# Performance work log

Measured on AMD Instinct MI355X. Metric: run time of the kernel, lower is better.

## Reference

```python
import jax, jax.numpy as jnp
import numpy as np

B, S, I, H, C = 32, 512, 768, 512, 10


def setup_inputs() -> dict:
    key = jax.random.key(0)
    ks = jax.random.split(key, 16)
    n = lambda k, shp, s=0.02: jax.random.normal(k, shp, dtype=jnp.float32) * s
    inp = {
        "sentence_embeds": jax.random.normal(ks[0], (B, S, I), dtype=jnp.float32),
        "Wenc": n(ks[1], (H, I)),
        "benc": jnp.zeros((H,), jnp.float32),
        "Wdec": n(ks[2], (H, H)),
        "bdec": jnp.zeros((H,), jnp.float32),
        "v": jax.random.uniform(ks[3], (H,), dtype=jnp.float32),
        "Wih_f": n(ks[4], (4 * H, 2 * I)),
        "Whh_f": n(ks[5], (4 * H, H)),
        "bih_f": jnp.zeros((4 * H,), jnp.float32),
        "bhh_f": jnp.zeros((4 * H,), jnp.float32),
        "Wih_b": n(ks[6], (4 * H, 2 * I)),
        "Whh_b": n(ks[7], (4 * H, H)),
        "bih_b": jnp.zeros((4 * H,), jnp.float32),
        "bhh_b": jnp.zeros((4 * H,), jnp.float32),
        "Wout": n(ks[8], (C, 2 * H)),
        "bout": jnp.zeros((C,), jnp.float32),
    }
    return inp


def _run_direction(embeds, enc_proj, Wdec, bdec, v, Wih, Whh, bih, bhh):
    # embeds: [B,S,I], enc_proj: [B,S,H]. Returns per-step hidden states [S,B,H].
    b = embeds.shape[0]
    h0 = jnp.zeros((b, H), embeds.dtype)
    c0 = jnp.zeros((b, H), embeds.dtype)

    def step(carry, x_t):
        h, c = carry
        # Bahdanau additive attention over all encoder positions
        dec = h @ Wdec.T + bdec                                   # [B,H]
        scores = jnp.einsum("h,bsh->bs", v, jnp.tanh(enc_proj + dec[:, None, :]))
        w = jax.nn.softmax(scores, axis=1)                        # [B,S]
        ctx = jnp.einsum("bs,bsi->bi", w, embeds)                 # [B,I]
        inp = jnp.concatenate([ctx, x_t], axis=1)                 # [B,2I]
        gates = inp @ Wih.T + h @ Whh.T + (bih + bhh)             # [B,4H]
        i, f, g, o = jnp.split(gates, 4, axis=1)                  # torch LSTM gate order
        c = jax.nn.sigmoid(f) * c + jax.nn.sigmoid(i) * jnp.tanh(g)
        h = jax.nn.sigmoid(o) * jnp.tanh(c)
        return (h, c), h

    xs = jnp.swapaxes(embeds, 0, 1)  # [S,B,I]
    _, hs = jax.lax.scan(step, (h0, c0), xs)
    return hs


def reference(sentence_embeds, Wenc, benc, Wdec, bdec, v, Wih_f, Whh_f, bih_f, bhh_f,
              Wih_b, Whh_b, bih_b, bhh_b, Wout, bout):
    # Encoder projection is loop-invariant in the original; compute once.
    enc_proj = sentence_embeds @ Wenc.T + benc  # [B,S,H]
    hs_f = _run_direction(sentence_embeds, enc_proj, Wdec, bdec, v, Wih_f, Whh_f, bih_f, bhh_f)
    hs_b = _run_direction(sentence_embeds[:, ::-1, :], enc_proj, Wdec, bdec, v, Wih_b, Whh_b, bih_b, bhh_b)
    hs_b = hs_b[::-1]                                             # align backward outputs to time order
    combined = jnp.concatenate([hs_f, hs_b], axis=-1)             # [S,B,2H]
    preds = combined @ Wout.T + bout                              # [S,B,C]
    return jnp.swapaxes(preds, 0, 1)                              # [B,S,C]
```

## Files before the change

### kernel.cpp

```cpp
#include <hip/hip_runtime.h>
#include <stdint.h>

#define DEVINL __device__ __forceinline__

constexpr int B_  = 32;
constexpr int S_  = 512;
constexpr int I_  = 768;
constexpr int H_  = 512;
constexpr int C_  = 10;
constexpr int R_  = 64;
constexpr int G4H = 2048;
constexpr int I2_ = 1536;

using bf16x8 = __attribute__((ext_vector_type(8))) short;
using f32x4  = __attribute__((ext_vector_type(4))) float;
typedef unsigned short u16;
typedef unsigned int   u32;

constexpr size_t OFF_TE   = 0;
constexpr size_t OFF_EMB  = OFF_TE   + (size_t)B_*S_*H_*2;
constexpr size_t OFF_WDEC = OFF_EMB  + (size_t)B_*S_*I_*2;
constexpr size_t OFF_WHH  = OFF_WDEC + (size_t)H_*H_*2;
constexpr size_t OFF_WIL  = OFF_WHH  + (size_t)2*G4H*H_*2;
constexpr size_t OFF_WIR  = OFF_WIL  + (size_t)2*G4H*I_*2;
constexpr size_t OFF_WENC = OFF_WIR  + (size_t)2*G4H*I_*2;
constexpr size_t OFF_H    = OFF_WENC + (size_t)H_*I_*2;
constexpr size_t OFF_C    = OFF_H    + (size_t)R_*H_*2;
constexpr size_t OFF_TD   = OFF_C    + (size_t)R_*H_*4;
constexpr size_t OFF_HWH  = OFF_TD   + (size_t)R_*H_*4;
constexpr size_t OFF_XW   = OFF_HWH  + (size_t)R_*G4H*4;
constexpr size_t OFF_CTX  = OFF_XW   + (size_t)R_*G4H*4;
constexpr size_t OFF_SUME = OFF_CTX  + (size_t)R_*I_*4;
constexpr size_t OFF_M    = OFF_SUME + 256;
constexpr size_t WS_NEED  = OFF_M + 256;

DEVINL float asf(u32 u){ union{u32 i; float f;} x; x.i=u; return x.f; }
DEVINL u32   asu(float f){ union{u32 i; float f;} x; x.f=f; return x.i; }
DEVINL float bf2f(u16 h){ return asf((u32)h << 16); }
DEVINL u16   f2bf(float f){ u32 u = asu(f); return (u16)((u + 0x7fffu + ((u>>16)&1u)) >> 16); }
DEVINL float frcp(float x){
#if __has_builtin(__builtin_amdgcn_rcpf)
  return __builtin_amdgcn_rcpf(x);
#else
  return 1.0f/x;
#endif
}
DEVINL float sigm(float x){ return frcp(1.0f + __expf(-x)); }

__global__ void k_setup(char* ws, const float* Wenc, const float* Wdec,
                        const float* Whh_f, const float* Whh_b,
                        const float* Wih_f, const float* Wih_b,
                        float* out){
  int tid = blockIdx.x*blockDim.x + threadIdx.x;
  int nth = gridDim.x*blockDim.x;
  for (int i = tid; i < B_*S_*C_; i += nth) out[i] = 0.f;
  u16* hB = (u16*)(ws+OFF_H);
  for (int i = tid; i < R_*H_; i += nth) hB[i] = 0;
  float* cS = (float*)(ws+OFF_C);
  for (int i = tid; i < R_*H_; i += nth) cS[i] = 0.f;
  float* mb = (float*)(ws+OFF_M);
  for (int i = tid; i < R_; i += nth) mb[i] = 0.f;
  u16* wd = (u16*)(ws+OFF_WDEC);
  for (int i = tid; i < H_*H_; i += nth) wd[i] = f2bf(Wdec[i]);
  u16* we = (u16*)(ws+OFF_WENC);
  for (int i = tid; i < H_*I_; i += nth) we[i] = f2bf(Wenc[i]);
  u16* wh = (u16*)(ws+OFF_WHH);
  for (int i = tid; i < G4H*H_; i += nth){
    wh[i] = f2bf(Whh_f[i]);
    wh[G4H*H_ + i] = f2bf(Whh_b[i]);
  }
  u16* wl = (u16*)(ws+OFF_WIL);
  u16* wr = (u16*)(ws+OFF_WIR);
  for (int i = tid; i < G4H*I_; i += nth){
    int n = i / I_, k = i - n*I_;
    wl[i]            = f2bf(Wih_f[n*I2_ + k]);
    wr[i]            = f2bf(Wih_f[n*I2_ + I_ + k]);
    wl[G4H*I_ + i]   = f2bf(Wih_b[n*I2_ + k]);
    wr[G4H*I_ + i]   = f2bf(Wih_b[n*I2_ + I_ + k]);
  }
}

__global__ void k_embconv(char* ws, const float* emb){
  u16* e = (u16*)(ws+OFF_EMB);
  int tid = blockIdx.x*blockDim.x + threadIdx.x;
  int nth = gridDim.x*blockDim.x;
  int n4 = (B_*S_*I_)/4;
  const float4* src = (const float4*)emb;
  ushort4* dst = (ushort4*)e;
  for (int i = tid; i < n4; i += nth){
    float4 x = src[i];
    ushort4 o;
    o.x = f2bf(x.x); o.y = f2bf(x.y); o.z = f2bf(x.z); o.w = f2bf(x.w);
    dst[i] = o;
  }
}

__global__ __launch_bounds__(256) void k_enc(char* ws, const float* benc){
  const u16* A = (const u16*)(ws+OFF_EMB);
  const u16* W = (const u16*)(ws+OFF_WENC);
  u16* Te = (u16*)(ws+OFF_TE);
  int wg = blockIdx.x;
  int mt = wg >> 3, ng = wg & 7;
  int wave = threadIdx.x >> 6, lane = threadIdx.x & 63;
  int m0 = mt*16, n0 = ng*64 + wave*16;
  int lr = lane & 15, lkb = (lane>>4)*8;
  const u16* ap = A + (size_t)(m0+lr)*I_ + lkb;
  const u16* bp = W + (size_t)(n0+lr)*I_ + lkb;
  f32x4 acc = {0.f,0.f,0.f,0.f};
  for (int k = 0; k < I_; k += 32){
    bf16x8 a = *(const bf16x8*)(ap + k);
    bf16x8 b = *(const bf16x8*)(bp + k);
    acc = __builtin_amdgcn_mfma_f32_16x16x32_bf16(a, b, acc, 0, 0, 0);
  }
  int row4 = (lane>>4)*4;
  #pragma unroll
  for (int q = 0; q < 4; q++){
    int rr = m0 + row4 + q, cc = n0 + lr;
    Te[(size_t)rr*H_ + cc] = f2bf(tanhf(acc[q] + benc[cc]));
  }
}

__global__ __launch_bounds__(256) void k_step1(char* ws, const float* bdec, int t){
  int wg = blockIdx.x;
  if (wg >= 288){
    int tid = (wg-288)*256 + threadIdx.x;
    float* ctx = (float*)(ws+OFF_CTX);
    for (int i = tid; i < R_*I_; i += 512) ctx[i] = 0.f;
    float* se = (float*)(ws+OFF_SUME);
    for (int i = tid; i < R_; i += 512) se[i] = 0.f;
    return;
  }
  int wave = threadIdx.x >> 6, lane = threadIdx.x & 63;
  int tile = wg*4 + wave;
  int lr = lane & 15, lkb = (lane>>4)*8, row4 = (lane>>4)*4;
  const u16* hB = (const u16*)(ws+OFF_H);
  f32x4 acc = {0.f,0.f,0.f,0.f};
  if (tile < 128){
    int m0 = (tile>>5)*16, n0 = (tile&31)*16;
    const u16* W = (const u16*)(ws+OFF_WDEC);
    const u16* ap = hB + (size_t)(m0+lr)*H_ + lkb;
    const u16* bp = W + (size_t)(n0+lr)*H_ + lkb;
    for (int k = 0; k < H_; k += 32){
      bf16x8 a = *(const bf16x8*)(ap + k);
      bf16x8 b = *(const bf16x8*)(bp + k);
      acc = __builtin_amdgcn_mfma_f32_16x16x32_bf16(a, b, acc, 0, 0, 0);
    }
    float* Td = (float*)(ws+OFF_TD);
    #pragma unroll
    for (int q = 0; q < 4; q++){
      int rr = m0 + row4 + q, cc = n0 + lr;
      Td[rr*H_ + cc] = tanhf(acc[q] + bdec[cc]);
    }
  } else if (tile < 640){
    int t2 = tile - 128; int dir = t2 >> 8; int t3 = t2 & 255;
    int m0 = dir*32 + (t3>>7)*16;
    int n0 = (t3 & 127)*16;
    const u16* W = (const u16*)(ws+OFF_WHH) + (size_t)dir*G4H*H_;
    const u16* ap = hB + (size_t)(m0+lr)*H_ + lkb;
    const u16* bp = W + (size_t)(n0+lr)*H_ + lkb;
    for (int k = 0; k < H_; k += 32){
      bf16x8 a = *(const bf16x8*)(ap + k);
      bf16x8 b = *(const bf16x8*)(bp + k);
      acc = __builtin_amdgcn_mfma_f32_16x16x32_bf16(a, b, acc, 0, 0, 0);
    }
    float* o = (float*)(ws+OFF_HWH);
    #pragma unroll
    for (int q = 0; q < 4; q++){
      int rr = m0 + row4 + q;
      o[(size_t)rr*G4H + n0 + lr] = acc[q];
    }
  } else {
    int t2 = tile - 640; int dir = t2 >> 8; int t3 = t2 & 255;
    int bbase = (t3>>7)*16;
    int n0 = (t3 & 127)*16;
    int trow = dir ? (S_-1-t) : t;
    const u16* E = (const u16*)(ws+OFF_EMB);
    const u16* W = (const u16*)(ws+OFF_WIR) + (size_t)dir*G4H*I_;
    const u16* ap = E + ((size_t)(bbase+lr)*S_ + trow)*I_ + lkb;
    const u16* bp = W + (size_t)(n0+lr)*I_ + lkb;
    for (int k = 0; k < I_; k += 32){
      bf16x8 a = *(const bf16x8*)(ap + k);
      bf16x8 b = *(const bf16x8*)(bp + k);
      acc = __builtin_amdgcn_mfma_f32_16x16x32_bf16(a, b, acc, 0, 0, 0);
    }
    float* o = (float*)(ws+OFF_XW);
    #pragma unroll
    for (int q = 0; q < 4; q++){
      int bb = bbase + row4 + q;
      o[(size_t)(dir*32+bb)*G4H + n0 + lr] = acc[q];
    }
  }
}

__global__ __launch_bounds__(512) void k_attn(char* ws, const float* v){
  int wg = blockIdx.x;
  int b = wg & 31, pair = wg >> 5;
  int s0A = pair*32, s0B = S_ - pair*32 - 32;
  int tid = threadIdx.x, lane = tid & 63, wave = tid >> 6;
  const u16* Te = (const u16*)(ws+OFF_TE);
  const float* Td = (const float*)(ws+OFF_TD);
  const float* mb = (const float*)(ws+OFF_M);
  __shared__ float ldsE[2][2][32];
  int h0 = lane*8;
  float tdf[8], tdb[8], va[8];
  #pragma unroll
  for (int j = 0; j < 8; j++){
    tdf[j] = Td[b*H_ + h0 + j];
    tdb[j] = Td[(32+b)*H_ + h0 + j];
    va[j]  = v[h0 + j];
  }
  float mF = mb[b], mB = mb[32+b];
  for (int r = wave; r < 64; r += 8){
    int ci = r >> 5, u = r & 31;
    int s = (ci ? s0B : s0A) + u;
    const uint4 tv = *(const uint4*)(Te + ((size_t)(b*S_ + s))*H_ + h0);
    u32 wv[4] = {tv.x, tv.y, tv.z, tv.w};
    float af = 0.f, ab = 0.f;
    #pragma unroll
    for (int q = 0; q < 4; q++){
      int j = 2*q;
      float te0 = asf(wv[q] << 16);
      float te1 = asf(wv[q] & 0xffff0000u);
      float d0f = fmaf(te0, tdf[j],   1.0f);
      float d0b = fmaf(te0, tdb[j],   1.0f);
      af = fmaf((te0+tdf[j])*frcp(d0f), va[j], af);
      ab = fmaf((te0+tdb[j])*frcp(d0b), va[j], ab);
      float d1f = fmaf(te1, tdf[j+1], 1.0f);
      float d1b = fmaf(te1, tdb[j+1], 1.0f);
      af = fmaf((te1+tdf[j+1])*frcp(d1f), va[j+1], af);
      ab = fmaf((te1+tdb[j+1])*frcp(d1b), va[j+1], ab);
    }
    #pragma unroll
    for (int off = 1; off < 64; off <<= 1){
      af += __shfl_xor(af, off);
      ab += __shfl_xor(ab, off);
    }
    float ef = __expf(fminf(fmaxf(af - mF, -80.f), 80.f));
    float eb = __expf(fminf(fmaxf(ab - mB, -80.f), 80.f));
    if (lane == 0){ ldsE[0][ci][u] = ef; ldsE[1][ci][u] = eb; }
  }
  __syncthreads();
  if (tid < 2){
    float s = 0.f;
    for (int ci = 0; ci < 2; ci++)
      for (int u = 0; u < 32; u++) s += ldsE[tid][ci][u];
    atomicAdd((float*)(ws+OFF_SUME) + tid*32 + b, s);
  }
  if (tid < 192){
    int i0 = tid*4;
    const u16* E = (const u16*)(ws+OFF_EMB);
    float cf[4] = {0.f,0.f,0.f,0.f}, cb[4] = {0.f,0.f,0.f,0.f};
    for (int hf = 0; hf < 2; hf++){
      int sbase = hf ? s0B : s0A;
      for (int u = 0; u < 32; u++){
        ushort4 x4 = *(const ushort4*)(E + ((size_t)(b*S_ + sbase + u))*I_ + i0);
        float wf = ldsE[0][hf][u];
        float wb = ldsE[1][1-hf][31-u];
        float x0 = bf2f(x4.x), x1 = bf2f(x4.y), x2 = bf2f(x4.z), x3 = bf2f(x4.w);
        cf[0] = fmaf(wf, x0, cf[0]); cf[1] = fmaf(wf, x1, cf[1]);
        cf[2] = fmaf(wf, x2, cf[2]); cf[3] = fmaf(wf, x3, cf[3]);
        cb[0] = fmaf(wb, x0, cb[0]); cb[1] = fmaf(wb, x1, cb[1]);
        cb[2] = fmaf(wb, x2, cb[2]); cb[3] = fmaf(wb, x3, cb[3]);
      }
    }
    float* ctx = (float*)(ws+OFF_CTX);
    #pragma unroll
    for (int z = 0; z < 4; z++){
      atomicAdd(&ctx[(size_t)b*I_ + i0 + z], cf[z]);
      atomicAdd(&ctx[(size_t)(32+b)*I_ + i0 + z], cb[z]);
    }
  }
}

__global__ __launch_bounds__(256) void k_upd(char* ws,
        const float* bih_f, const float* bhh_f,
        const float* bih_b, const float* bhh_b,
        const float* Wout, const float* bout,
        float* out, int t){
  int wg = blockIdx.x;
  int dir = wg >> 5, hc = wg & 31;
  int tid = threadIdx.x, lane = tid & 63, gt = tid >> 6;
  __shared__ u16 Abuf[32][776];
  __shared__ float Gs[4][32][16];
  __shared__ float Hb[32][16];
  __shared__ float ldsInv[32];
  const float* ctx = (const float*)(ws+OFF_CTX) + (size_t)dir*32*I_;
  const float* se  = (const float*)(ws+OFF_SUME) + dir*32;
  if (tid < 32) ldsInv[tid] = 1.0f / fmaxf(se[tid], 1e-30f);
  __syncthreads();
  for (int idx = tid; idx < 32*I_; idx += 256){
    int bb = idx / I_, k = idx - bb*I_;
    Abuf[bb][k] = f2bf(ctx[(size_t)bb*I_ + k] * ldsInv[bb]);
  }
  __syncthreads();
  int lr = lane & 15, lkb = (lane>>4)*8, row4 = (lane>>4)*4;
  const u16* W = (const u16*)(ws+OFF_WIL) + (size_t)dir*G4H*I_;
  int n_g = gt*512 + hc*16 + lr;
  const u16* bp = W + (size_t)n_g*I_ + lkb;
  f32x4 acc0 = {0.f,0.f,0.f,0.f}, acc1 = {0.f,0.f,0.f,0.f};
  for (int k = 0; k < I_; k += 32){
    bf16x8 av0 = *(const bf16x8*)(&Abuf[lr][k + lkb]);
    bf16x8 av1 = *(const bf16x8*)(&Abuf[16 + lr][k + lkb]);
    bf16x8 bv  = *(const bf16x8*)(bp + k);
    acc0 = __builtin_amdgcn_mfma_f32_16x16x32_bf16(av0, bv, acc0, 0, 0, 0);
    acc1 = __builtin_amdgcn_mfma_f32_16x16x32_bf16(av1, bv, acc1, 0, 0, 0);
  }
  const float* xW = (const float*)(ws+OFF_XW);
  const float* hW = (const float*)(ws+OFF_HWH);
  const float* bih = dir ? bih_b : bih_f;
  const float* bhh = dir ? bhh_b : bhh_f;
  #pragma unroll
  for (int q = 0; q < 4; q++){
    int bb = row4 + q; int rr = dir*32 + bb;
    Gs[gt][bb][lr] = acc0[q] + xW[(size_t)rr*G4H + n_g] + hW[(size_t)rr*G4H + n_g]
                   + bih[n_g] + bhh[n_g];
  }
  #pragma unroll
  for (int q = 0; q < 4; q++){
    int bb = 16 + row4 + q; int rr = dir*32 + bb;
    Gs[gt][bb][lr] = acc1[q] + xW[(size_t)rr*G4H + n_g] + hW[(size_t)rr*G4H + n_g]
                   + bih[n_g] + bhh[n_g];
  }
  __syncthreads();
  float* cS = (float*)(ws+OFF_C);
  u16* hB = (u16*)(ws+OFF_H);
  for (int ci = tid; ci < 512; ci += 256){
    int bb = ci >> 4, j = ci & 15;
    int hg = hc*16 + j, rr = dir*32 + bb;
    float ig = sigm(Gs[0][bb][j]);
    float fg = sigm(Gs[1][bb][j]);
    float gg = tanhf(Gs[2][bb][j]);
    float og = sigm(Gs[3][bb][j]);
    float cn = fmaf(fg, cS[(size_t)rr*H_ + hg], ig*gg);
    float hn = og * tanhf(cn);
    cS[(size_t)rr*H_ + hg] = cn;
    hB[(size_t)rr*H_ + hg] = f2bf(hn);
    Hb[bb][j] = hn;
  }
  __syncthreads();
  for (int idx = tid; idx < 320; idx += 256){
    int bb = idx / 10, cc = idx - bb*10;
    const float* wr = Wout + (size_t)cc*1024 + dir*512 + hc*16;
    float s = 0.f;
    #pragma unroll
    for (int j = 0; j < 16; j++) s = fmaf(Hb[bb][j], wr[j], s);
    if (dir == 0 && hc == 0) s += bout[cc];
    int st = dir ? (S_-1-t) : t;
    atomicAdd(&out[((size_t)bb*S_ + st)*C_ + cc], s);
  }
  if (hc == 0 && tid < 32){
    float* mbp = (float*)(ws+OFF_M);
    mbp[dir*32 + tid] += logf(fmaxf(se[tid], 1e-30f));
  }
}

extern "C" void kernel_launch(void* const* d_in, const int* in_sizes, int n_in,
                              void* d_out, int out_size, void* d_ws, size_t ws_size,
                              hipStream_t stream){
  const float* emb   = (const float*)d_in[0];
  const float* Wenc  = (const float*)d_in[1];
  const float* benc  = (const float*)d_in[2];
  const float* Wdec  = (const float*)d_in[3];
  const float* bdec  = (const float*)d_in[4];
  const float* v     = (const float*)d_in[5];
  const float* Wih_f = (const float*)d_in[6];
  const float* Whh_f = (const float*)d_in[7];
  const float* bih_f = (const float*)d_in[8];
  const float* bhh_f = (const float*)d_in[9];
  const float* Wih_b = (const float*)d_in[10];
  const float* Whh_b = (const float*)d_in[11];
  const float* bih_b = (const float*)d_in[12];
  const float* bhh_b = (const float*)d_in[13];
  const float* Wout  = (const float*)d_in[14];
  const float* bout  = (const float*)d_in[15];
  float* out = (float*)d_out;
  char* ws = (char*)d_ws;
  if (ws_size < WS_NEED) return;

  k_setup<<<dim3(512), dim3(256), 0, stream>>>(ws, Wenc, Wdec, Whh_f, Whh_b, Wih_f, Wih_b, out);
  k_embconv<<<dim3(2048), dim3(256), 0, stream>>>(ws, emb);
  k_enc<<<dim3(8192), dim3(256), 0, stream>>>(ws, benc);
  for (int t = 0; t < S_; t++){
    k_step1<<<dim3(290), dim3(256), 0, stream>>>(ws, bdec, t);
    k_attn<<<dim3(256), dim3(512), 0, stream>>>(ws, v);
    k_upd<<<dim3(64), dim3(256), 0, stream>>>(ws, bih_f, bhh_f, bih_b, bhh_b, Wout, bout, out, t);
  }
}
```

Measured before the change: 25.09 ms.

## Fuse per-step kernels into one persistent kernel with software grid barriers

Replaces the 1536 per-timestep kernel launches (step1, attn, upd) with a single persistent kernel of 256 blocks that loops over all 512 timesteps and separates phases with an atomic-counter grid barrier. The LSTM update is respread over 256 blocks of 8 batch rows each, and xW/hW preloading runs concurrently with the MFMA on spare waves. The attention context sum splits the two halves across more threads and merges them in LDS before the atomics. This removes launch overhead but relies on all 256 blocks being co-resident, and spin-wait barriers add latency of their own.

```diff
diff --git a/kernel.cpp b/kernel.cpp
--- a/kernel.cpp
+++ b/kernel.cpp
@@ -11,6 +11,8 @@
 constexpr int R_  = 64;
 constexpr int G4H = 2048;
 constexpr int I2_ = 1536;
+constexpr int NBLK = 256;
+constexpr int NTHR = 512;
 
 using bf16x8 = __attribute__((ext_vector_type(8))) short;
 using f32x4  = __attribute__((ext_vector_type(4))) float;
@@ -32,7 +34,8 @@
 constexpr size_t OFF_CTX  = OFF_XW   + (size_t)R_*G4H*4;
 constexpr size_t OFF_SUME = OFF_CTX  + (size_t)R_*I_*4;
 constexpr size_t OFF_M    = OFF_SUME + 256;
-constexpr size_t WS_NEED  = OFF_M + 256;
+constexpr size_t OFF_BAR  = OFF_M    + 256;
+constexpr size_t WS_NEED  = OFF_BAR + 64;
 
 DEVINL float asf(u32 u){ union{u32 i; float f;} x; x.i=u; return x.f; }
 DEVINL u32   asu(float f){ union{u32 i; float f;} x; x.f=f; return x.i; }
@@ -46,6 +49,30 @@
 #endif
 }
 DEVINL float sigm(float x){ return frcp(1.0f + __expf(-x)); }
+
+DEVINL void gridbar(u32* bar){
+  __syncthreads();
+  if (threadIdx.x == 0){
+    u32 g = __hip_atomic_load(bar+1, __ATOMIC_RELAXED, __HIP_MEMORY_SCOPE_AGENT);
+    __threadfence();
+    u32 a = __hip_atomic_fetch_add(bar, 1u, __ATOMIC_RELAXED, __HIP_MEMORY_SCOPE_AGENT);
+    if (a == (u32)NBLK-1u){
+      __hip_atomic_store(bar, 0u, __ATOMIC_RELAXED, __HIP_MEMORY_SCOPE_AGENT);
+      __threadfence();
+      __hip_atomic_store(bar+1, g+1u, __ATOMIC_RELAXED, __HIP_MEMORY_SCOPE_AGENT);
+    } else {
+      while (__hip_atomic_load(bar+1, __ATOMIC_RELAXED, __HIP_MEMORY_SCOPE_AGENT) == g)
+        __builtin_amdgcn_s_sleep(2);
+    }
+    __threadfence();
+  }
+  __syncthreads();
+}
+
+struct SMemB { float ldsE[2][2][32]; float cpart[192][8]; };
+struct SMemC { u16 Abuf[16][776]; float Gpre[4][8][16]; float Gs[4][8][16];
+               float Hb[8][16]; float inv[8]; float sum[8]; };
+union alignas(16) SMem { SMemB b; SMemC c; };
 
 __global__ void k_setup(char* ws, const float* Wenc, const float* Wdec,
                         const float* Whh_f, const float* Whh_b,
@@ -60,6 +87,8 @@
   for (int i = tid; i < R_*H_; i += nth) cS[i] = 0.f;
   float* mb = (float*)(ws+OFF_M);
   for (int i = tid; i < R_; i += nth) mb[i] = 0.f;
+  u32* bar = (u32*)(ws+OFF_BAR);
+  if (tid < 2) bar[tid] = 0u;
   u16* wd = (u16*)(ws+OFF_WDEC);
   for (int i = tid; i < H_*H_; i += nth) wd[i] = f2bf(Wdec[i]);
   u16* we = (u16*)(ws+OFF_WENC);
@@ -120,237 +149,264 @@
   }
 }
 
-__global__ __launch_bounds__(256) void k_step1(char* ws, const float* bdec, int t){
-  int wg = blockIdx.x;
-  if (wg >= 288){
-    int tid = (wg-288)*256 + threadIdx.x;
-    float* ctx = (float*)(ws+OFF_CTX);
-    for (int i = tid; i < R_*I_; i += 512) ctx[i] = 0.f;
-    float* se = (float*)(ws+OFF_SUME);
-    for (int i = tid; i < R_; i += 512) se[i] = 0.f;
-    return;
-  }
-  int wave = threadIdx.x >> 6, lane = threadIdx.x & 63;
-  int tile = wg*4 + wave;
-  int lr = lane & 15, lkb = (lane>>4)*8, row4 = (lane>>4)*4;
-  const u16* hB = (const u16*)(ws+OFF_H);
-  f32x4 acc = {0.f,0.f,0.f,0.f};
-  if (tile < 128){
-    int m0 = (tile>>5)*16, n0 = (tile&31)*16;
-    const u16* W = (const u16*)(ws+OFF_WDEC);
-    const u16* ap = hB + (size_t)(m0+lr)*H_ + lkb;
-    const u16* bp = W + (size_t)(n0+lr)*H_ + lkb;
-    for (int k = 0; k < H_; k += 32){
-      bf16x8 a = *(const bf16x8*)(ap + k);
-      bf16x8 b = *(const bf16x8*)(bp + k);
-      acc = __builtin_amdgcn_mfma_f32_16x16x32_bf16(a, b, acc, 0, 0, 0);
-    }
-    float* Td = (float*)(ws+OFF_TD);
-    #pragma unroll
-    for (int q = 0; q < 4; q++){
-      int rr = m0 + row4 + q, cc = n0 + lr;
-      Td[rr*H_ + cc] = tanhf(acc[q] + bdec[cc]);
-    }
-  } else if (tile < 640){
-    int t2 = tile - 128; int dir = t2 >> 8; int t3 = t2 & 255;
-    int m0 = dir*32 + (t3>>7)*16;
-    int n0 = (t3 & 127)*16;
-    const u16* W = (const u16*)(ws+OFF_WHH) + (size_t)dir*G4H*H_;
-    const u16* ap = hB + (size_t)(m0+lr)*H_ + lkb;
-    const u16* bp = W + (size_t)(n0+lr)*H_ + lkb;
-    for (int k = 0; k < H_; k += 32){
-      bf16x8 a = *(const bf16x8*)(ap + k);
-      bf16x8 b = *(const bf16x8*)(bp + k);
-      acc = __builtin_amdgcn_mfma_f32_16x16x32_bf16(a, b, acc, 0, 0, 0);
-    }
-    float* o = (float*)(ws+OFF_HWH);
-    #pragma unroll
-    for (int q = 0; q < 4; q++){
-      int rr = m0 + row4 + q;
-      o[(size_t)rr*G4H + n0 + lr] = acc[q];
-    }
-  } else {
-    int t2 = tile - 640; int dir = t2 >> 8; int t3 = t2 & 255;
-    int bbase = (t3>>7)*16;
-    int n0 = (t3 & 127)*16;
-    int trow = dir ? (S_-1-t) : t;
-    const u16* E = (const u16*)(ws+OFF_EMB);
-    const u16* W = (const u16*)(ws+OFF_WIR) + (size_t)dir*G4H*I_;
-    const u16* ap = E + ((size_t)(bbase+lr)*S_ + trow)*I_ + lkb;
-    const u16* bp = W + (size_t)(n0+lr)*I_ + lkb;
-    for (int k = 0; k < I_; k += 32){
-      bf16x8 a = *(const bf16x8*)(ap + k);
-      bf16x8 b = *(const bf16x8*)(bp + k);
-      acc = __builtin_amdgcn_mfma_f32_16x16x32_bf16(a, b, acc, 0, 0, 0);
-    }
-    float* o = (float*)(ws+OFF_XW);
-    #pragma unroll
-    for (int q = 0; q < 4; q++){
-      int bb = bbase + row4 + q;
-      o[(size_t)(dir*32+bb)*G4H + n0 + lr] = acc[q];
-    }
-  }
-}
-
-__global__ __launch_bounds__(512) void k_attn(char* ws, const float* v){
-  int wg = blockIdx.x;
-  int b = wg & 31, pair = wg >> 5;
-  int s0A = pair*32, s0B = S_ - pair*32 - 32;
-  int tid = threadIdx.x, lane = tid & 63, wave = tid >> 6;
-  const u16* Te = (const u16*)(ws+OFF_TE);
-  const float* Td = (const float*)(ws+OFF_TD);
-  const float* mb = (const float*)(ws+OFF_M);
-  __shared__ float ldsE[2][2][32];
-  int h0 = lane*8;
-  float tdf[8], tdb[8], va[8];
-  #pragma unroll
-  for (int j = 0; j < 8; j++){
-    tdf[j] = Td[b*H_ + h0 + j];
-    tdb[j] = Td[(32+b)*H_ + h0 + j];
-    va[j]  = v[h0 + j];
-  }
-  float mF = mb[b], mB = mb[32+b];
-  for (int r = wave; r < 64; r += 8){
-    int ci = r >> 5, u = r & 31;
-    int s = (ci ? s0B : s0A) + u;
-    const uint4 tv = *(const uint4*)(Te + ((size_t)(b*S_ + s))*H_ + h0);
-    u32 wv[4] = {tv.x, tv.y, tv.z, tv.w};
-    float af = 0.f, ab = 0.f;
-    #pragma unroll
-    for (int q = 0; q < 4; q++){
-      int j = 2*q;
-      float te0 = asf(wv[q] << 16);
-      float te1 = asf(wv[q] & 0xffff0000u);
-      float d0f = fmaf(te0, tdf[j],   1.0f);
-      float d0b = fmaf(te0, tdb[j],   1.0f);
-      af = fmaf((te0+tdf[j])*frcp(d0f), va[j], af);
-      ab = fmaf((te0+tdb[j])*frcp(d0b), va[j], ab);
-      float d1f = fmaf(te1, tdf[j+1], 1.0f);
-      float d1b = fmaf(te1, tdb[j+1], 1.0f);
-      af = fmaf((te1+tdf[j+1])*frcp(d1f), va[j+1], af);
-      ab = fmaf((te1+tdb[j+1])*frcp(d1b), va[j+1], ab);
-    }
-    #pragma unroll
-    for (int off = 1; off < 64; off <<= 1){
-      af += __shfl_xor(af, off);
-      ab += __shfl_xor(ab, off);
-    }
-    float ef = __expf(fminf(fmaxf(af - mF, -80.f), 80.f));
-    float eb = __expf(fminf(fmaxf(ab - mB, -80.f), 80.f));
-    if (lane == 0){ ldsE[0][ci][u] = ef; ldsE[1][ci][u] = eb; }
-  }
-  __syncthreads();
-  if (tid < 2){
-    float s = 0.f;
-    for (int ci = 0; ci < 2; ci++)
-      for (int u = 0; u < 32; u++) s += ldsE[tid][ci][u];
-    atomicAdd((float*)(ws+OFF_SUME) + tid*32 + b, s);
-  }
-  if (tid < 192){
-    int i0 = tid*4;
-    const u16* E = (const u16*)(ws+OFF_EMB);
-    float cf[4] = {0.f,0.f,0.f,0.f}, cb[4] = {0.f,0.f,0.f,0.f};
-    for (int hf = 0; hf < 2; hf++){
-      int sbase = hf ? s0B : s0A;
-      for (int u = 0; u < 32; u++){
-        ushort4 x4 = *(const ushort4*)(E + ((size_t)(b*S_ + sbase + u))*I_ + i0);
-        float wf = ldsE[0][hf][u];
-        float wb = ldsE[1][1-hf][31-u];
-        float x0 = bf2f(x4.x), x1 = bf2f(x4.y), x2 = bf2f(x4.z), x3 = bf2f(x4.w);
-        cf[0] = fmaf(wf, x0, cf[0]); cf[1] = fmaf(wf, x1, cf[1]);
-        cf[2] = fmaf(wf, x2, cf[2]); cf[3] = fmaf(wf, x3, cf[3]);
-        cb[0] = fmaf(wb, x0, cb[0]); cb[1] = fmaf(wb, x1, cb[1]);
-        cb[2] = fmaf(wb, x2, cb[2]); cb[3] = fmaf(wb, x3, cb[3]);
-      }
-    }
-    float* ctx = (float*)(ws+OFF_CTX);
-    #pragma unroll
-    for (int z = 0; z < 4; z++){
-      atomicAdd(&ctx[(size_t)b*I_ + i0 + z], cf[z]);
-      atomicAdd(&ctx[(size_t)(32+b)*I_ + i0 + z], cb[z]);
-    }
-  }
-}
-
-__global__ __launch_bounds__(256) void k_upd(char* ws,
+__global__ __launch_bounds__(NTHR) void k_persist(char* ws,
+        const float* bdec, const float* v,
         const float* bih_f, const float* bhh_f,
         const float* bih_b, const float* bhh_b,
-        const float* Wout, const float* bout,
-        float* out, int t){
-  int wg = blockIdx.x;
-  int dir = wg >> 5, hc = wg & 31;
-  int tid = threadIdx.x, lane = tid & 63, gt = tid >> 6;
-  __shared__ u16 Abuf[32][776];
-  __shared__ float Gs[4][32][16];
-  __shared__ float Hb[32][16];
-  __shared__ float ldsInv[32];
-  const float* ctx = (const float*)(ws+OFF_CTX) + (size_t)dir*32*I_;
-  const float* se  = (const float*)(ws+OFF_SUME) + dir*32;
-  if (tid < 32) ldsInv[tid] = 1.0f / fmaxf(se[tid], 1e-30f);
+        const float* Wout, const float* bout, float* out){
+  __shared__ SMem sh;
+  u32* bar = (u32*)(ws+OFF_BAR);
+  const int tid = threadIdx.x, lane = tid & 63, wave = tid >> 6;
+  const int lr = lane & 15, lkb = (lane>>4)*8, row4 = (lane>>4)*4;
+
+  for (int i = tid; i < 16*776; i += NTHR) ((u16*)sh.c.Abuf)[i] = 0;
   __syncthreads();
-  for (int idx = tid; idx < 32*I_; idx += 256){
-    int bb = idx / I_, k = idx - bb*I_;
-    Abuf[bb][k] = f2bf(ctx[(size_t)bb*I_ + k] * ldsInv[bb]);
-  }
-  __syncthreads();
-  int lr = lane & 15, lkb = (lane>>4)*8, row4 = (lane>>4)*4;
-  const u16* W = (const u16*)(ws+OFF_WIL) + (size_t)dir*G4H*I_;
-  int n_g = gt*512 + hc*16 + lr;
-  const u16* bp = W + (size_t)n_g*I_ + lkb;
-  f32x4 acc0 = {0.f,0.f,0.f,0.f}, acc1 = {0.f,0.f,0.f,0.f};
-  for (int k = 0; k < I_; k += 32){
-    bf16x8 av0 = *(const bf16x8*)(&Abuf[lr][k + lkb]);
-    bf16x8 av1 = *(const bf16x8*)(&Abuf[16 + lr][k + lkb]);
-    bf16x8 bv  = *(const bf16x8*)(bp + k);
-    acc0 = __builtin_amdgcn_mfma_f32_16x16x32_bf16(av0, bv, acc0, 0, 0, 0);
-    acc1 = __builtin_amdgcn_mfma_f32_16x16x32_bf16(av1, bv, acc1, 0, 0, 0);
-  }
-  const float* xW = (const float*)(ws+OFF_XW);
-  const float* hW = (const float*)(ws+OFF_HWH);
-  const float* bih = dir ? bih_b : bih_f;
-  const float* bhh = dir ? bhh_b : bhh_f;
-  #pragma unroll
-  for (int q = 0; q < 4; q++){
-    int bb = row4 + q; int rr = dir*32 + bb;
-    Gs[gt][bb][lr] = acc0[q] + xW[(size_t)rr*G4H + n_g] + hW[(size_t)rr*G4H + n_g]
-                   + bih[n_g] + bhh[n_g];
-  }
-  #pragma unroll
-  for (int q = 0; q < 4; q++){
-    int bb = 16 + row4 + q; int rr = dir*32 + bb;
-    Gs[gt][bb][lr] = acc1[q] + xW[(size_t)rr*G4H + n_g] + hW[(size_t)rr*G4H + n_g]
-                   + bih[n_g] + bhh[n_g];
-  }
-  __syncthreads();
-  float* cS = (float*)(ws+OFF_C);
-  u16* hB = (u16*)(ws+OFF_H);
-  for (int ci = tid; ci < 512; ci += 256){
-    int bb = ci >> 4, j = ci & 15;
-    int hg = hc*16 + j, rr = dir*32 + bb;
-    float ig = sigm(Gs[0][bb][j]);
-    float fg = sigm(Gs[1][bb][j]);
-    float gg = tanhf(Gs[2][bb][j]);
-    float og = sigm(Gs[3][bb][j]);
-    float cn = fmaf(fg, cS[(size_t)rr*H_ + hg], ig*gg);
-    float hn = og * tanhf(cn);
-    cS[(size_t)rr*H_ + hg] = cn;
-    hB[(size_t)rr*H_ + hg] = f2bf(hn);
-    Hb[bb][j] = hn;
-  }
-  __syncthreads();
-  for (int idx = tid; idx < 320; idx += 256){
-    int bb = idx / 10, cc = idx - bb*10;
-    const float* wr = Wout + (size_t)cc*1024 + dir*512 + hc*16;
-    float s = 0.f;
-    #pragma unroll
-    for (int j = 0; j < 16; j++) s = fmaf(Hb[bb][j], wr[j], s);
-    if (dir == 0 && hc == 0) s += bout[cc];
-    int st = dir ? (S_-1-t) : t;
-    atomicAdd(&out[((size_t)bb*S_ + st)*C_ + cc], s);
-  }
-  if (hc == 0 && tid < 32){
-    float* mbp = (float*)(ws+OFF_M);
-    mbp[dir*32 + tid] += logf(fmaxf(se[tid], 1e-30f));
+
+  for (int t = 0; t < S_; ++t){
+    {
+      int gw = blockIdx.x*8 + wave;
+      const u16* hB = (const u16*)(ws+OFF_H);
+      if (gw < 128){
+        int m0 = (gw>>5)*16, n0 = (gw&31)*16;
+        const u16* W = (const u16*)(ws+OFF_WDEC);
+        const u16* ap = hB + (size_t)(m0+lr)*H_ + lkb;
+        const u16* bp = W + (size_t)(n0+lr)*H_ + lkb;
+        f32x4 acc = {0.f,0.f,0.f,0.f};
+        for (int k = 0; k < H_; k += 32){
+          bf16x8 a = *(const bf16x8*)(ap + k);
+          bf16x8 b = *(const bf16x8*)(bp + k);
+          acc = __builtin_amdgcn_mfma_f32_16x16x32_bf16(a, b, acc, 0, 0, 0);
+        }
+        float* Td = (float*)(ws+OFF_TD);
+        #pragma unroll
+        for (int q = 0; q < 4; q++){
+          int rr = m0 + row4 + q, cc = n0 + lr;
+          Td[rr*H_ + cc] = tanhf(acc[q] + bdec[cc]);
+        }
+      } else if (gw < 640){
+        int t2 = gw - 128; int dir = t2 >> 8; int t3 = t2 & 255;
+        int m0 = dir*32 + (t3>>7)*16;
+        int n0 = (t3 & 127)*16;
+        const u16* W = (const u16*)(ws+OFF_WHH) + (size_t)dir*G4H*H_;
+        const u16* ap = hB + (size_t)(m0+lr)*H_ + lkb;
+        const u16* bp = W + (size_t)(n0+lr)*H_ + lkb;
+        f32x4 acc = {0.f,0.f,0.f,0.f};
+        for (int k = 0; k < H_; k += 32){
+          bf16x8 a = *(const bf16x8*)(ap + k);
+          bf16x8 b = *(const bf16x8*)(bp + k);
+          acc = __builtin_amdgcn_mfma_f32_16x16x32_bf16(a, b, acc, 0, 0, 0);
+        }
+        float* o = (float*)(ws+OFF_HWH);
+        #pragma unroll
+        for (int q = 0; q < 4; q++){
+          int rr = m0 + row4 + q;
+          o[(size_t)rr*G4H + n0 + lr] = acc[q];
+        }
+      } else if (gw < 1152){
+        int t2 = gw - 640; int dir = t2 >> 8; int t3 = t2 & 255;
+        int bbase = (t3>>7)*16;
+        int n0 = (t3 & 127)*16;
+        int trow = dir ? (S_-1-t) : t;
+        const u16* E = (const u16*)(ws+OFF_EMB);
+        const u16* W = (const u16*)(ws+OFF_WIR) + (size_t)dir*G4H*I_;
+        const u16* ap = E + ((size_t)(bbase+lr)*S_ + trow)*I_ + lkb;
+        const u16* bp = W + (size_t)(n0+lr)*I_ + lkb;
+        f32x4 acc = {0.f,0.f,0.f,0.f};
+        for (int k = 0; k < I_; k += 32){
+          bf16x8 a = *(const bf16x8*)(ap + k);
+          bf16x8 b = *(const bf16x8*)(bp + k);
+          acc = __builtin_amdgcn_mfma_f32_16x16x32_bf16(a, b, acc, 0, 0, 0);
+        }
+        float* o = (float*)(ws+OFF_XW);
+        #pragma unroll
+        for (int q = 0; q < 4; q++){
+          int bb = bbase + row4 + q;
+          o[(size_t)(dir*32+bb)*G4H + n0 + lr] = acc[q];
+        }
+      } else {
+        int zid = (gw - 1152)*64 + lane;
+        float* ctx = (float*)(ws+OFF_CTX);
+        if (zid < R_*I_) ctx[zid] = 0.f;
+        if (zid < R_) ((float*)(ws+OFF_SUME))[zid] = 0.f;
+      }
+    }
+    gridbar(bar);
+    {
+      int wg = blockIdx.x;
+      int b = wg & 31, pair = wg >> 5;
+      int s0A = pair*32, s0B = S_ - pair*32 - 32;
+      const u16* Te = (const u16*)(ws+OFF_TE);
+      const float* Td = (const float*)(ws+OFF_TD);
+      const float* mbp = (const float*)(ws+OFF_M);
+      int h0 = lane*8;
+      float tdf[8], tdb[8], va[8];
+      #pragma unroll
+      for (int j = 0; j < 8; j++){
+        tdf[j] = Td[b*H_ + h0 + j];
+        tdb[j] = Td[(32+b)*H_ + h0 + j];
+        va[j]  = v[h0 + j];
+      }
+      float mF = mbp[b], mB = mbp[32+b];
+      #pragma unroll 2
+      for (int r = wave; r < 64; r += 8){
+        int ci = r >> 5, u = r & 31;
+        int s = (ci ? s0B : s0A) + u;
+        const uint4 tv = *(const uint4*)(Te + ((size_t)(b*S_ + s))*H_ + h0);
+        u32 wv[4] = {tv.x, tv.y, tv.z, tv.w};
+        float af = 0.f, ab = 0.f;
+        #pragma unroll
+        for (int q = 0; q < 4; q++){
+          int j = 2*q;
+          float te0 = asf(wv[q] << 16);
+          float te1 = asf(wv[q] & 0xffff0000u);
+          float d0f = fmaf(te0, tdf[j],   1.0f);
+          float d0b = fmaf(te0, tdb[j],   1.0f);
+          af = fmaf((te0+tdf[j])*frcp(d0f), va[j], af);
+          ab = fmaf((te0+tdb[j])*frcp(d0b), va[j], ab);
+          float d1f = fmaf(te1, tdf[j+1], 1.0f);
+          float d1b = fmaf(te1, tdb[j+1], 1.0f);
+          af = fmaf((te1+tdf[j+1])*frcp(d1f), va[j+1], af);
+          ab = fmaf((te1+tdb[j+1])*frcp(d1b), va[j+1], ab);
+        }
+        #pragma unroll
+        for (int off = 1; off < 64; off <<= 1){
+          af += __shfl_xor(af, off);
+          ab += __shfl_xor(ab, off);
+        }
+        float ef = __expf(fminf(fmaxf(af - mF, -80.f), 80.f));
+        float eb = __expf(fminf(fmaxf(ab - mB, -80.f), 80.f));
+        if (lane == 0){ sh.b.ldsE[0][ci][u] = ef; sh.b.ldsE[1][ci][u] = eb; }
+      }
+      __syncthreads();
+      if (tid < 2){
+        float s = 0.f;
+        for (int ci = 0; ci < 2; ci++)
+          for (int u = 0; u < 32; u++) s += sh.b.ldsE[tid][ci][u];
+        atomicAdd((float*)(ws+OFF_SUME) + tid*32 + b, s);
+      }
+      float cf[4] = {0.f,0.f,0.f,0.f}, cb[4] = {0.f,0.f,0.f,0.f};
+      if (tid < 384){
+        int hf = (tid >= 192) ? 1 : 0;
+        int t2 = hf ? tid-192 : tid;
+        int i0 = t2*4;
+        const u16* E = (const u16*)(ws+OFF_EMB);
+        int sbase = hf ? s0B : s0A;
+        #pragma unroll 4
+        for (int u = 0; u < 32; u++){
+          ushort4 x4 = *(const ushort4*)(E + ((size_t)(b*S_ + sbase + u))*I_ + i0);
+          float wf = sh.b.ldsE[0][hf][u];
+          float wb = sh.b.ldsE[1][1-hf][31-u];
+          float x0 = bf2f(x4.x), x1 = bf2f(x4.y), x2 = bf2f(x4.z), x3 = bf2f(x4.w);
+          cf[0] = fmaf(wf, x0, cf[0]); cf[1] = fmaf(wf, x1, cf[1]);
+          cf[2] = fmaf(wf, x2, cf[2]); cf[3] = fmaf(wf, x3, cf[3]);
+          cb[0] = fmaf(wb, x0, cb[0]); cb[1] = fmaf(wb, x1, cb[1]);
+          cb[2] = fmaf(wb, x2, cb[2]); cb[3] = fmaf(wb, x3, cb[3]);
+        }
+        if (hf){
+          #pragma unroll
+          for (int z = 0; z < 4; z++){
+            sh.b.cpart[t2][z]   = cf[z];
+            sh.b.cpart[t2][4+z] = cb[z];
+          }
+        }
+      }
+      __syncthreads();
+      if (tid < 192){
+        float* ctx = (float*)(ws+OFF_CTX);
+        int i0 = tid*4;
+        #pragma unroll
+        for (int z = 0; z < 4; z++){
+          atomicAdd(&ctx[(size_t)b*I_ + i0 + z],      cf[z] + sh.b.cpart[tid][z]);
+          atomicAdd(&ctx[(size_t)(32+b)*I_ + i0 + z], cb[z] + sh.b.cpart[tid][4+z]);
+        }
+      }
+    }
+    gridbar(bar);
+    {
+      int blk = blockIdx.x;
+      int dir = blk >> 7, rest = blk & 127, hc = rest >> 2, qb = rest & 3;
+      int rb0 = qb*8;
+      const float* se = (const float*)(ws+OFF_SUME) + dir*32;
+      if (tid < 8){
+        float s_ = se[rb0 + tid];
+        sh.c.sum[tid] = s_;
+        sh.c.inv[tid] = 1.0f / fmaxf(s_, 1e-30f);
+      }
+      __syncthreads();
+      const float* ctx = (const float*)(ws+OFF_CTX) + (size_t)dir*32*I_;
+      for (int idx = tid; idx < 8*I_; idx += NTHR){
+        int j = idx / I_, k = idx - j*I_;
+        sh.c.Abuf[j][k] = f2bf(ctx[(size_t)(rb0+j)*I_ + k] * sh.c.inv[j]);
+      }
+      __syncthreads();
+      f32x4 acc = {0.f,0.f,0.f,0.f};
+      if (wave < 4){
+        int gt = wave;
+        const u16* Wp = (const u16*)(ws+OFF_WIL) + (size_t)dir*G4H*I_;
+        int n_g = gt*512 + hc*16 + lr;
+        const u16* bp = Wp + (size_t)n_g*I_ + lkb;
+        for (int k = 0; k < I_; k += 32){
+          bf16x8 av = *(const bf16x8*)(&sh.c.Abuf[lr][k + lkb]);
+          bf16x8 bv = *(const bf16x8*)(bp + k);
+          acc = __builtin_amdgcn_mfma_f32_16x16x32_bf16(av, bv, acc, 0, 0, 0);
+        }
+      } else {
+        int gt = wave - 4;
+        const float* xW = (const float*)(ws+OFF_XW);
+        const float* hW = (const float*)(ws+OFF_HWH);
+        const float* bih = dir ? bih_b : bih_f;
+        const float* bhh = dir ? bhh_b : bhh_f;
+        int j0 = lane >> 4, col = lane & 15;
+        int n = gt*512 + hc*16 + col;
+        #pragma unroll
+        for (int jj = j0; jj < 8; jj += 4){
+          size_t rr = (size_t)(dir*32 + rb0 + jj);
+          sh.c.Gpre[gt][jj][col] = xW[rr*G4H + n] + hW[rr*G4H + n] + bih[n] + bhh[n];
+        }
+      }
+      __syncthreads();
+      if (wave < 4){
+        int gt = wave, col = lane & 15;
+        #pragma unroll
+        for (int q = 0; q < 4; q++){
+          int row = row4 + q;
+          if (row < 8) sh.c.Gs[gt][row][col] = acc[q] + sh.c.Gpre[gt][row][col];
+        }
+      }
+      __syncthreads();
+      float* cS = (float*)(ws+OFF_C);
+      u16* hBw = (u16*)(ws+OFF_H);
+      if (tid < 128){
+        int j = tid >> 4, col = tid & 15;
+        int hg = hc*16 + col;
+        size_t rr = (size_t)(dir*32 + rb0 + j);
+        float ig = sigm(sh.c.Gs[0][j][col]);
+        float fg = sigm(sh.c.Gs[1][j][col]);
+        float gg = tanhf(sh.c.Gs[2][j][col]);
+        float og = sigm(sh.c.Gs[3][j][col]);
+        float cn = fmaf(fg, cS[rr*H_ + hg], ig*gg);
+        float hn = og * tanhf(cn);
+        cS[rr*H_ + hg] = cn;
+        hBw[rr*H_ + hg] = f2bf(hn);
+        sh.c.Hb[j][col] = hn;
+      }
+      __syncthreads();
+      if (tid < 80){
+        int bb = tid/10, cc = tid - bb*10;
+        const float* wr = Wout + (size_t)cc*1024 + dir*512 + hc*16;
+        float s = 0.f;
+        #pragma unroll
+        for (int j = 0; j < 16; j++) s = fmaf(sh.c.Hb[bb][j], wr[j], s);
+        if (dir == 0 && hc == 0) s += bout[cc];
+        int st = dir ? (S_-1-t) : t;
+        atomicAdd(&out[((size_t)(qb*8+bb)*S_ + st)*C_ + cc], s);
+      }
+      if (hc == 0 && tid < 8){
+        float* mbp = (float*)(ws+OFF_M);
+        mbp[dir*32 + rb0 + tid] += logf(fmaxf(sh.c.sum[tid], 1e-30f));
+      }
+    }
+    gridbar(bar);
   }
 }
 
@@ -380,9 +436,6 @@
   k_setup<<<dim3(512), dim3(256), 0, stream>>>(ws, Wenc, Wdec, Whh_f, Whh_b, Wih_f, Wih_b, out);
   k_embconv<<<dim3(2048), dim3(256), 0, stream>>>(ws, emb);
   k_enc<<<dim3(8192), dim3(256), 0, stream>>>(ws, benc);
-  for (int t = 0; t < S_; t++){
-    k_step1<<<dim3(290), dim3(256), 0, stream>>>(ws, bdec, t);
-    k_attn<<<dim3(256), dim3(512), 0, stream>>>(ws, v);
-    k_upd<<<dim3(64), dim3(256), 0, stream>>>(ws, bih_f, bhh_f, bih_b, bhh_b, Wout, bout, out, t);
-  }
-}
+  k_persist<<<dim3(NBLK), dim3(NTHR), 0, stream>>>(ws, bdec, v,
+      bih_f, bhh_f, bih_b, bhh_b, Wout, bout, out);
+}
```

New measurement: 61.54 ms. +145.3%, slower.
